# Optimization experiments

Hardware: AMD Instinct MI355X
Metric: run time of the kernel (lower is better)

## Reference

```python
import jax, jax.numpy as jnp
import numpy as np

NUM_CLASSES = 1000
TEMPERATURE = 0.1
B, B_OOD, D = 4096, 4096, 512


def _l2norm(x):
    return x / jnp.linalg.norm(x, axis=-1, keepdims=True)


def setup_inputs() -> dict:
    key = jax.random.key(0)
    k1, k2, k3, k4, k5 = jax.random.split(key, 5)
    return {
        "centers1": _l2norm(jax.random.normal(k1, (NUM_CLASSES, D), dtype=jnp.float32)),
        "features": _l2norm(jax.random.normal(k2, (B, D), dtype=jnp.float32)),
        "targets": jax.random.randint(k3, (B,), 0, NUM_CLASSES, dtype=jnp.int64 if jax.config.jax_enable_x64 else jnp.int32),
        "features_ood": _l2norm(jax.random.normal(k4, (B_OOD, D), dtype=jnp.float32)),
        "pseudo_target_ood": jax.random.randint(k5, (B_OOD,), 0, NUM_CLASSES, dtype=jnp.int64 if jax.config.jax_enable_x64 else jnp.int32),
    }


def reference(centers1, features, targets, features_ood, pseudo_target_ood):
    C = centers1.shape[0]
    b = features.shape[0]
    bo = features_ood.shape[0]
    n = b + C + bo  # total anchors: batch + class centers + ood

    centers_lbl = jnp.arange(C, dtype=targets.dtype)
    ood_lbl = jnp.full((bo,), C, dtype=targets.dtype)  # ood gets label == num_classes
    targets_all = jnp.concatenate([targets, centers_lbl, ood_lbl])              # [N]
    targets_all_class = jnp.concatenate([targets, centers_lbl, pseudo_target_ood])  # [N]

    # per-class count over all N labels (pseudo labels for ood)
    batch_cls_count = jnp.zeros((C,), dtype=jnp.float32).at[targets_all_class].add(1.0)

    # positive mask: same label as anchor, excluding self (diagonal for j < B)
    mask = (targets_all[:b, None] == targets_all[None, :]).astype(jnp.float32)  # [B,N]
    logits_mask = 1.0 - (jnp.arange(n)[None, :] == jnp.arange(b)[:, None]).astype(jnp.float32)
    mask = mask * logits_mask

    features_all = jnp.concatenate([features, centers1, features_ood], axis=0)  # [N,D]
    logits = jnp.matmul(features, features_all.T) / TEMPERATURE                 # [B,N]
    logits = logits - jax.lax.stop_gradient(jnp.max(logits, axis=1, keepdims=True))

    exp_logits = jnp.exp(logits) * logits_mask
    # class-balanced per-instance weight (count of the column's class, minus positive mask)
    per_ins_weight = batch_cls_count[targets_all_class][None, :] - mask         # [B,N]
    exp_logits_sum = jnp.sum(exp_logits / per_ins_weight, axis=1, keepdims=True)
    log_prob = logits - jnp.log(exp_logits_sum)

    mean_log_prob_pos = jnp.sum(mask * log_prob, axis=1) / jnp.sum(mask, axis=1)
    loss = -jnp.mean(mean_log_prob_pos)
    return loss
```

## Files before the change

kernel.cpp:

```cpp
#include <hip/hip_runtime.h>
#include <stdint.h>

#define NUM_C 1000
#define NB    4096
#define NCOL  9192
#define NPAD  9216
#define DK    512
#define BM    128
#define BN    256
#define INV_T 10.0f

typedef __attribute__((ext_vector_type(16))) float f32x16;
typedef __attribute__((ext_vector_type(8)))  int   i32x8;

#define OFF_FALL  0u
#define OFF_CNT   4718592u
#define OFF_CNTT  4722688u
#define OFF_S     4726784u
#define OFF_P     4743168u

__device__ __forceinline__ void async16(const void* g, void* l) {
  __builtin_amdgcn_global_load_lds((const __attribute__((address_space(1))) void*)g,
                                   (__attribute__((address_space(3))) void*)l,
                                   16, 0, 0);
}

__device__ __forceinline__ unsigned sw_e4m3(float x) {
  float ax = fabsf(x);
  unsigned s = (__float_as_uint(x) >> 24) & 0x80u;
  if (ax < 0.015625f) {
    int n = (int)rintf(ax * 512.0f);
    if (n >= 8) return s | 0x08u;
    return s | (unsigned)n;
  }
  if (ax >= 448.0f) return s | 0x7Eu;
  unsigned u = __float_as_uint(ax);
  int ee = (int)(u >> 23) - 127;
  float scale = __uint_as_float((unsigned)(3 - ee + 127) << 23);
  int qv = (int)rintf(ax * scale);
  if (qv == 16) { ee++; qv = 8; }
  return s | (unsigned)(((ee + 7) << 3) | (qv - 8));
}

template <bool HI>
__device__ __forceinline__ int cvt2(float a, float b, int old) {
#if __has_builtin(__builtin_amdgcn_cvt_pk_fp8_f32)
  return __builtin_amdgcn_cvt_pk_fp8_f32(a, b, old, HI);
#else
  unsigned pk = sw_e4m3(a) | (sw_e4m3(b) << 8);
  return HI ? (int)(((unsigned)old & 0x0000FFFFu) | (pk << 16))
            : (int)(((unsigned)old & 0xFFFF0000u) | pk);
#endif
}

__device__ __forceinline__ i32x8 mk8(uint4 lo, uint4 hi) {
  i32x8 r;
  r[0] = (int)lo.x; r[1] = (int)lo.y; r[2] = (int)lo.z; r[3] = (int)lo.w;
  r[4] = (int)hi.x; r[5] = (int)hi.y; r[6] = (int)hi.z; r[7] = (int)hi.w;
  return r;
}

#define MFMA_SC(a, b, c) \
  __builtin_amdgcn_mfma_scale_f32_32x32x64_f8f6f4((a), (b), (c), 0, 0, 0, 0x7F7F7F7F, 0, 0x7F7F7F7F)

__global__ __launch_bounds__(256) void prep_k(const float* __restrict__ centers,
                                              const float* __restrict__ feats,
                                              const float* __restrict__ ood,
                                              const int* __restrict__ targets,
                                              const int* __restrict__ pseudo,
                                              uint4* __restrict__ fall,
                                              unsigned* __restrict__ cnt,
                                              unsigned* __restrict__ cntT,
                                              float* __restrict__ SP) {
  __shared__ unsigned hc[1024];
  __shared__ unsigned hct[1024];
  const int tid = threadIdx.x;

  int idx  = blockIdx.x * 256 + tid;
  int tile = idx >> 10;
  int kq   = (idx >> 7) & 7;
  int p    = idx & 127;
  int c    = p ^ ((p >> 3) & 7);
  int lane = c >> 1;
  int row  = tile * 32 + (lane & 31);
  int k0   = kq * 64 + (lane >> 5) * 32 + (c & 1) * 16;

  const float* src = nullptr;
  if (row < NB)              src = feats   + (size_t)row * DK;
  else if (row < NB + NUM_C) src = centers + (size_t)(row - NB) * DK;
  else if (row < NCOL)       src = ood     + (size_t)(row - NB - NUM_C) * DK;
  uint4 out = make_uint4(0u, 0u, 0u, 0u);
  if (src) {
    float4 v0 = *(const float4*)(src + k0);
    float4 v1 = *(const float4*)(src + k0 + 4);
    float4 v2 = *(const float4*)(src + k0 + 8);
    float4 v3 = *(const float4*)(src + k0 + 12);
    int q;
    q = 0; q = cvt2<false>(v0.x, v0.y, q); q = cvt2<true>(v0.z, v0.w, q); out.x = (unsigned)q;
    q = 0; q = cvt2<false>(v1.x, v1.y, q); q = cvt2<true>(v1.z, v1.w, q); out.y = (unsigned)q;
    q = 0; q = cvt2<false>(v2.x, v2.y, q); q = cvt2<true>(v2.z, v2.w, q); out.z = (unsigned)q;
    q = 0; q = cvt2<false>(v3.x, v3.y, q); q = cvt2<true>(v3.z, v3.w, q); out.w = (unsigned)q;
  }
  fall[idx] = out;

  if (blockIdx.x < 16) {
    for (int kk = tid; kk < 1024; kk += 256) { hc[kk] = 0u; hct[kk] = 0u; }
    __syncthreads();
    int i = blockIdx.x * 256 + tid;
    int tt = targets[i];
    atomicAdd(&hc[tt], 1u);
    atomicAdd(&hct[tt], 1u);
    atomicAdd(&hc[pseudo[i]], 1u);
    __syncthreads();
    for (int kk = tid; kk < 1024; kk += 256) {
      unsigned cc = hc[kk], ct = hct[kk];
      if (cc) atomicAdd(&cnt[kk], cc);
      if (ct) atomicAdd(&cntT[kk], ct);
    }
  } else if (blockIdx.x < 48) {
    SP[(blockIdx.x - 16) * 256 + tid] = 0.0f;
  }
}

__global__ __launch_bounds__(256, 2) void gemm_fused(const unsigned char* __restrict__ fall,
                                                     const int* __restrict__ targets,
                                                     const int* __restrict__ pseudo,
                                                     const unsigned* __restrict__ cnt,
                                                     float* __restrict__ Sacc,
                                                     float* __restrict__ Pacc) {
  __shared__ unsigned char Alds[65536];
  __shared__ int    sLbl[BN];
  __shared__ float  sRw0[BN];
  __shared__ float  sRw1[BN];
  __shared__ int    sTgt[BM];

  const int tid  = threadIdx.x;
  int flat = (int)blockIdx.y * 36 + (int)blockIdx.x;
  int swz  = (flat & 7) * 144 + (flat >> 3);
  const int nTile = swz >> 5;
  const int mTile = swz & 31;
  const int lane  = tid & 63;
  const int wv    = tid >> 6;

  {
    const unsigned char* aSrc = fall + (size_t)mTile * 65536;
#pragma unroll
    for (int i = 0; i < 16; i++)
      async16(aSrc + (i * 256 + tid) * 16, &Alds[(i * 256 + tid) * 16]);
  }

  {
    int j = nTile * BN + tid;
    int lbl, tac;
    if (j >= NCOL)         { lbl = -1; tac = -1; }
    else if (j < NB)       { tac = targets[j]; lbl = tac; }
    else if (j < NB+NUM_C) { tac = j - NB;     lbl = tac; }
    else                   { tac = pseudo[j - NB - NUM_C]; lbl = NUM_C; }
    sLbl[tid] = lbl;
    if (tac >= 0) {
      float w = (float)(1u + cnt[tac]);
      sRw0[tid] = 1.0f / w;
      sRw1[tid] = 1.0f / (w - 1.0f);
    } else {
      sRw0[tid] = 0.f;
      sRw1[tid] = 0.f;
    }
    if (tid < BM) sTgt[tid] = targets[mTile * BM + tid];
  }

  f32x16 acc[4][2];
  {
    f32x16 z;
#pragma unroll
    for (int t = 0; t < 16; t++) z[t] = 0.f;
#pragma unroll
    for (int mi = 0; mi < 4; mi++) { acc[mi][0] = z; acc[mi][1] = z; }
  }

  const int swzo = ((lane >> 2) & 7) << 4;
  const int off0 = (lane << 5) ^ swzo;
  const int off1 = off0 ^ 16;

  const unsigned char* bBase0 = fall + (size_t)(nTile * 8 + wv * 2) * 16384;
  const unsigned char* bBase1 = bBase0 + 16384;

  uint4 b0l = *(const uint4*)(bBase0 + off0);
  uint4 b0h = *(const uint4*)(bBase0 + off1);
  uint4 b1l = *(const uint4*)(bBase1 + off0);
  uint4 b1h = *(const uint4*)(bBase1 + off1);

  __syncthreads();

#pragma unroll
  for (int kq = 0; kq < 8; kq++) {
    uint4 n0l, n0h, n1l, n1h;
    if (kq < 7) {
      const unsigned char* pb0 = bBase0 + (kq + 1) * 2048;
      const unsigned char* pb1 = bBase1 + (kq + 1) * 2048;
      n0l = *(const uint4*)(pb0 + off0); n0h = *(const uint4*)(pb0 + off1);
      n1l = *(const uint4*)(pb1 + off0); n1h = *(const uint4*)(pb1 + off1);
    }
    i32x8 bf0 = mk8(b0l, b0h);
    i32x8 bf1 = mk8(b1l, b1h);
#pragma unroll
    for (int mi = 0; mi < 4; mi++) {
      const unsigned ao = (unsigned)mi * 16384u + (unsigned)kq * 2048u;
      uint4 al = *(const uint4*)&Alds[ao + off0];
      uint4 ah = *(const uint4*)&Alds[ao + off1];
      i32x8 af = mk8(al, ah);
      acc[mi][0] = MFMA_SC(af, bf0, acc[mi][0]);
      acc[mi][1] = MFMA_SC(af, bf1, acc[mi][1]);
    }
    if (kq < 7) { b0l = n0l; b0h = n0h; b1l = n1l; b1h = n1h; }
  }

  const int cq = lane & 31;
  const int hh = lane >> 5;
  const int jl0 = wv * 64 + cq;
  const int jl1 = jl0 + 32;
  const int jg0 = nTile * BN + jl0;
  const int jg1 = jg0 + 32;
  const int lbl0 = sLbl[jl0], lbl1 = sLbl[jl1];
  const float w00 = sRw0[jl0], w01 = sRw1[jl0];
  const float w10 = sRw0[jl1], w11 = sRw1[jl1];

#define RED(m, s, h)                                           \
  {                                                            \
    float sS = (lane & (m)) ? vS[(s)] : vS[(s) + (h)];         \
    float sP = (lane & (m)) ? vP[(s)] : vP[(s) + (h)];         \
    float rS = __shfl_xor(sS, (m), 64);                        \
    float rP = __shfl_xor(sP, (m), 64);                        \
    vS[(s)] = ((lane & (m)) ? vS[(s) + (h)] : vS[(s)]) + rS;   \
    vP[(s)] = ((lane & (m)) ? vP[(s) + (h)] : vP[(s)]) + rP;   \
  }

#pragma unroll
  for (int mi = 0; mi < 4; mi++) {
    float vS[16], vP[16];
#pragma unroll
    for (int r = 0; r < 16; r++) {
      int rowT = (r & 3) + 8 * (r >> 2) + 4 * hh;
      int iloc = mi * 32 + rowT;
      int ig   = mTile * BM + iloc;
      int ti   = sTgt[iloc];
      float l0 = acc[mi][0][r] * INV_T;
      float l1 = acc[mi][1][r] * INV_T;
      bool d0 = (jg0 == ig), d1 = (jg1 == ig);
      bool p0 = (lbl0 == ti) && !d0;
      bool p1 = (lbl1 == ti) && !d1;
      float r0 = d0 ? 0.f : (p0 ? w01 : w00);
      float r1 = d1 ? 0.f : (p1 ? w11 : w10);
      vS[r] = __expf(l0 - 10.0f) * r0 + __expf(l1 - 10.0f) * r1;
      vP[r] = (p0 ? l0 : 0.f) + (p1 ? l1 : 0.f);
    }
    RED(1, 0, 8) RED(1, 1, 8) RED(1, 2, 8) RED(1, 3, 8)
    RED(1, 4, 8) RED(1, 5, 8) RED(1, 6, 8) RED(1, 7, 8)
    RED(2, 0, 4) RED(2, 1, 4) RED(2, 2, 4) RED(2, 3, 4)
    RED(4, 0, 2) RED(4, 1, 2)
    RED(8, 0, 1)
    vS[0] += __shfl_xor(vS[0], 16, 64);
    vP[0] += __shfl_xor(vP[0], 16, 64);
    if (!(lane & 16)) {
      int rr   = ((lane & 1) << 3) | ((lane & 2) << 1) | ((lane & 4) >> 1) | ((lane & 8) >> 3);
      int rowT = (rr & 3) + 8 * (rr >> 2) + 4 * hh;
      int ig   = mTile * BM + mi * 32 + rowT;
      atomicAdd(&Sacc[ig], vS[0]);
      atomicAdd(&Pacc[ig], vP[0]);
    }
  }
#undef RED
}

__global__ __launch_bounds__(256) void finalize_k(const float* __restrict__ S,
                                                  const float* __restrict__ P,
                                                  const int* __restrict__ targets,
                                                  const unsigned* __restrict__ cntT,
                                                  float* __restrict__ out) {
  __shared__ unsigned ct[1024];
  __shared__ float red[4];
  int tid = threadIdx.x;
  for (int k = tid; k < 1024; k += 256) ct[k] = cntT[k];
  __syncthreads();
  float local = 0.f;
  for (int i = tid; i < NB; i += 256) {
    float npos = (float)ct[targets[i]];
    local += P[i] / npos - INV_T - __logf(S[i]);
  }
  for (int m = 1; m < 64; m <<= 1) local += __shfl_xor(local, m, 64);
  if ((tid & 63) == 0) red[tid >> 6] = local;
  __syncthreads();
  if (tid == 0) {
    float t = red[0] + red[1] + red[2] + red[3];
    out[0] = -t / (float)NB;
  }
}

extern "C" void kernel_launch(void* const* d_in, const int* in_sizes, int n_in,
                              void* d_out, int out_size, void* d_ws, size_t ws_size,
                              hipStream_t stream) {
  const float* centers = (const float*)d_in[0];
  const float* feats   = (const float*)d_in[1];
  const int*   targets = (const int*)d_in[2];
  const float* ood     = (const float*)d_in[3];
  const int*   pseudo  = (const int*)d_in[4];

  char* ws = (char*)d_ws;
  uint4*    fall  = (uint4*)(ws + OFF_FALL);
  unsigned* cnt   = (unsigned*)(ws + OFF_CNT);
  unsigned* cntT  = (unsigned*)(ws + OFF_CNTT);
  float*    Sacc  = (float*)(ws + OFF_S);
  float*    Pacc  = (float*)(ws + OFF_P);

  hipMemsetAsync(ws + OFF_CNT, 0, 8192, stream);
  prep_k<<<dim3((NPAD * 32) / 256), 256, 0, stream>>>(centers, feats, ood, targets, pseudo,
                                                      fall, cnt, cntT, Sacc);
  gemm_fused<<<dim3(NPAD / BN, NB / BM), 256, 0, stream>>>((const unsigned char*)fall, targets,
                                                           pseudo, cnt, Sacc, Pacc);
  finalize_k<<<1, 256, 0, stream>>>(Sacc, Pacc, targets, cntT, (float*)d_out);
}
```

Measured before the change: 119.5 us.

## Fold finalize into GEMM via last-block counter, drop memset, use LDS row reduction

Drops the hipMemsetAsync and the separate finalize kernel. The GEMM blocks now bump a global done counter, and the last block to finish computes the loss. The class histogram is built by one dedicated block that writes counts directly, with no global atomics. Per-row partial sums are first reduced in LDS before one global atomic per row, and the MFMA loop runs at raised wave priority. This cuts launch overhead and global atomic traffic, at the cost of a serial single-block histogram and a threadfence per block.

```diff
diff --git a/kernel.cpp b/kernel.cpp
--- a/kernel.cpp
+++ b/kernel.cpp
@@ -18,6 +18,9 @@
 #define OFF_CNTT  4722688u
 #define OFF_S     4726784u
 #define OFF_P     4743168u
+#define OFF_DONE  4759552u
+
+#define NCHUNKBLK 1152
 
 __device__ __forceinline__ void async16(const void* g, void* l) {
   __builtin_amdgcn_global_load_lds((const __attribute__((address_space(1))) void*)g,
@@ -71,54 +74,57 @@
                                               uint4* __restrict__ fall,
                                               unsigned* __restrict__ cnt,
                                               unsigned* __restrict__ cntT,
-                                              float* __restrict__ SP) {
+                                              float* __restrict__ SP,
+                                              unsigned* __restrict__ done) {
   __shared__ unsigned hc[1024];
   __shared__ unsigned hct[1024];
   const int tid = threadIdx.x;
 
-  int idx  = blockIdx.x * 256 + tid;
-  int tile = idx >> 10;
-  int kq   = (idx >> 7) & 7;
-  int p    = idx & 127;
-  int c    = p ^ ((p >> 3) & 7);
-  int lane = c >> 1;
-  int row  = tile * 32 + (lane & 31);
-  int k0   = kq * 64 + (lane >> 5) * 32 + (c & 1) * 16;
-
-  const float* src = nullptr;
-  if (row < NB)              src = feats   + (size_t)row * DK;
-  else if (row < NB + NUM_C) src = centers + (size_t)(row - NB) * DK;
-  else if (row < NCOL)       src = ood     + (size_t)(row - NB - NUM_C) * DK;
-  uint4 out = make_uint4(0u, 0u, 0u, 0u);
-  if (src) {
-    float4 v0 = *(const float4*)(src + k0);
-    float4 v1 = *(const float4*)(src + k0 + 4);
-    float4 v2 = *(const float4*)(src + k0 + 8);
-    float4 v3 = *(const float4*)(src + k0 + 12);
-    int q;
-    q = 0; q = cvt2<false>(v0.x, v0.y, q); q = cvt2<true>(v0.z, v0.w, q); out.x = (unsigned)q;
-    q = 0; q = cvt2<false>(v1.x, v1.y, q); q = cvt2<true>(v1.z, v1.w, q); out.y = (unsigned)q;
-    q = 0; q = cvt2<false>(v2.x, v2.y, q); q = cvt2<true>(v2.z, v2.w, q); out.z = (unsigned)q;
-    q = 0; q = cvt2<false>(v3.x, v3.y, q); q = cvt2<true>(v3.z, v3.w, q); out.w = (unsigned)q;
-  }
-  fall[idx] = out;
-
-  if (blockIdx.x < 16) {
+  if (blockIdx.x < NCHUNKBLK) {
+    int idx  = blockIdx.x * 256 + tid;
+    int tile = idx >> 10;
+    int kq   = (idx >> 7) & 7;
+    int p    = idx & 127;
+    int c    = p ^ ((p >> 3) & 7);
+    int lane = c >> 1;
+    int row  = tile * 32 + (lane & 31);
+    int k0   = kq * 64 + (lane >> 5) * 32 + (c & 1) * 16;
+
+    const float* src = nullptr;
+    if (row < NB)              src = feats   + (size_t)row * DK;
+    else if (row < NB + NUM_C) src = centers + (size_t)(row - NB) * DK;
+    else if (row < NCOL)       src = ood     + (size_t)(row - NB - NUM_C) * DK;
+    uint4 out = make_uint4(0u, 0u, 0u, 0u);
+    if (src) {
+      float4 v0 = *(const float4*)(src + k0);
+      float4 v1 = *(const float4*)(src + k0 + 4);
+      float4 v2 = *(const float4*)(src + k0 + 8);
+      float4 v3 = *(const float4*)(src + k0 + 12);
+      int q;
+      q = 0; q = cvt2<false>(v0.x, v0.y, q); q = cvt2<true>(v0.z, v0.w, q); out.x = (unsigned)q;
+      q = 0; q = cvt2<false>(v1.x, v1.y, q); q = cvt2<true>(v1.z, v1.w, q); out.y = (unsigned)q;
+      q = 0; q = cvt2<false>(v2.x, v2.y, q); q = cvt2<true>(v2.z, v2.w, q); out.z = (unsigned)q;
+      q = 0; q = cvt2<false>(v3.x, v3.y, q); q = cvt2<true>(v3.z, v3.w, q); out.w = (unsigned)q;
+    }
+    fall[idx] = out;
+
+    if (blockIdx.x < 32)
+      SP[blockIdx.x * 256 + tid] = 0.0f;
+  } else {
     for (int kk = tid; kk < 1024; kk += 256) { hc[kk] = 0u; hct[kk] = 0u; }
     __syncthreads();
-    int i = blockIdx.x * 256 + tid;
-    int tt = targets[i];
-    atomicAdd(&hc[tt], 1u);
-    atomicAdd(&hct[tt], 1u);
-    atomicAdd(&hc[pseudo[i]], 1u);
+    for (int i = tid; i < NB; i += 256) {
+      int tt = targets[i];
+      atomicAdd(&hc[tt], 1u);
+      atomicAdd(&hct[tt], 1u);
+      atomicAdd(&hc[pseudo[i]], 1u);
+    }
     __syncthreads();
     for (int kk = tid; kk < 1024; kk += 256) {
-      unsigned cc = hc[kk], ct = hct[kk];
-      if (cc) atomicAdd(&cnt[kk], cc);
-      if (ct) atomicAdd(&cntT[kk], ct);
-    }
-  } else if (blockIdx.x < 48) {
-    SP[(blockIdx.x - 16) * 256 + tid] = 0.0f;
+      cnt[kk]  = hc[kk];
+      cntT[kk] = hct[kk];
+    }
+    if (tid == 0) *done = 0u;
   }
 }
 
@@ -126,13 +132,18 @@
                                                      const int* __restrict__ targets,
                                                      const int* __restrict__ pseudo,
                                                      const unsigned* __restrict__ cnt,
+                                                     const unsigned* __restrict__ cntT,
                                                      float* __restrict__ Sacc,
-                                                     float* __restrict__ Pacc) {
+                                                     float* __restrict__ Pacc,
+                                                     unsigned* __restrict__ done,
+                                                     float* __restrict__ out) {
   __shared__ unsigned char Alds[65536];
   __shared__ int    sLbl[BN];
   __shared__ float  sRw0[BN];
   __shared__ float  sRw1[BN];
   __shared__ int    sTgt[BM];
+  __shared__ unsigned sDone;
+  __shared__ float  red2[4];
 
   const int tid  = threadIdx.x;
   int flat = (int)blockIdx.y * 36 + (int)blockIdx.x;
@@ -191,6 +202,7 @@
 
   __syncthreads();
 
+  __builtin_amdgcn_s_setprio(1);
 #pragma unroll
   for (int kq = 0; kq < 8; kq++) {
     uint4 n0l, n0h, n1l, n1h;
@@ -213,6 +225,7 @@
     }
     if (kq < 7) { b0l = n0l; b0h = n0h; b1l = n1l; b1h = n1h; }
   }
+  __builtin_amdgcn_s_setprio(0);
 
   const int cq = lane & 31;
   const int hh = lane >> 5;
@@ -224,12 +237,18 @@
   const float w00 = sRw0[jl0], w01 = sRw1[jl0];
   const float w10 = sRw0[jl1], w11 = sRw1[jl1];
 
+  float* sS = (float*)Alds;
+  float* sP = (float*)(Alds + 512);
+  __syncthreads();
+  if (tid < BM) { sS[tid] = 0.f; sP[tid] = 0.f; }
+  __syncthreads();
+
 #define RED(m, s, h)                                           \
   {                                                            \
-    float sS = (lane & (m)) ? vS[(s)] : vS[(s) + (h)];         \
-    float sP = (lane & (m)) ? vP[(s)] : vP[(s) + (h)];         \
-    float rS = __shfl_xor(sS, (m), 64);                        \
-    float rP = __shfl_xor(sP, (m), 64);                        \
+    float sSv = (lane & (m)) ? vS[(s)] : vS[(s) + (h)];        \
+    float sPv = (lane & (m)) ? vP[(s)] : vP[(s) + (h)];        \
+    float rS = __shfl_xor(sSv, (m), 64);                       \
+    float rP = __shfl_xor(sPv, (m), 64);                       \
     vS[(s)] = ((lane & (m)) ? vS[(s) + (h)] : vS[(s)]) + rS;   \
     vP[(s)] = ((lane & (m)) ? vP[(s) + (h)] : vP[(s)]) + rP;   \
   }
@@ -258,40 +277,43 @@
     RED(2, 0, 4) RED(2, 1, 4) RED(2, 2, 4) RED(2, 3, 4)
     RED(4, 0, 2) RED(4, 1, 2)
     RED(8, 0, 1)
-    vS[0] += __shfl_xor(vS[0], 16, 64);
-    vP[0] += __shfl_xor(vP[0], 16, 64);
-    if (!(lane & 16)) {
+    {
       int rr   = ((lane & 1) << 3) | ((lane & 2) << 1) | ((lane & 4) >> 1) | ((lane & 8) >> 3);
       int rowT = (rr & 3) + 8 * (rr >> 2) + 4 * hh;
-      int ig   = mTile * BM + mi * 32 + rowT;
-      atomicAdd(&Sacc[ig], vS[0]);
-      atomicAdd(&Pacc[ig], vP[0]);
+      int iloc = mi * 32 + rowT;
+      atomicAdd(&sS[iloc], vS[0]);
+      atomicAdd(&sP[iloc], vP[0]);
     }
   }
 #undef RED
-}
-
-__global__ __launch_bounds__(256) void finalize_k(const float* __restrict__ S,
-                                                  const float* __restrict__ P,
-                                                  const int* __restrict__ targets,
-                                                  const unsigned* __restrict__ cntT,
-                                                  float* __restrict__ out) {
-  __shared__ unsigned ct[1024];
-  __shared__ float red[4];
-  int tid = threadIdx.x;
-  for (int k = tid; k < 1024; k += 256) ct[k] = cntT[k];
-  __syncthreads();
-  float local = 0.f;
-  for (int i = tid; i < NB; i += 256) {
-    float npos = (float)ct[targets[i]];
-    local += P[i] / npos - INV_T - __logf(S[i]);
-  }
-  for (int m = 1; m < 64; m <<= 1) local += __shfl_xor(local, m, 64);
-  if ((tid & 63) == 0) red[tid >> 6] = local;
-  __syncthreads();
-  if (tid == 0) {
-    float t = red[0] + red[1] + red[2] + red[3];
-    out[0] = -t / (float)NB;
+
+  __syncthreads();
+  if (tid < BM) {
+    int ig = mTile * BM + tid;
+    atomicAdd(&Sacc[ig], sS[tid]);
+    atomicAdd(&Pacc[ig], sP[tid]);
+  }
+
+  __threadfence();
+  if (tid == 0) sDone = (atomicAdd(done, 1u) == (unsigned)(36 * 32 - 1)) ? 1u : 0u;
+  __syncthreads();
+  if (sDone) {
+    unsigned* ct = (unsigned*)(Alds + 4096);
+    for (int k = tid; k < 1024; k += 256) ct[k] = cntT[k];
+    __syncthreads();
+    float local = 0.f;
+    for (int i = tid; i < NB; i += 256) {
+      float Sv = atomicAdd(&Sacc[i], 0.0f);
+      float Pv = atomicAdd(&Pacc[i], 0.0f);
+      local += Pv / (float)ct[targets[i]] - INV_T - __logf(Sv);
+    }
+    for (int m = 1; m < 64; m <<= 1) local += __shfl_xor(local, m, 64);
+    if ((tid & 63) == 0) red2[tid >> 6] = local;
+    __syncthreads();
+    if (tid == 0) {
+      float t = red2[0] + red2[1] + red2[2] + red2[3];
+      out[0] = -t / (float)NB;
+    }
   }
 }
 
@@ -310,11 +332,11 @@
   unsigned* cntT  = (unsigned*)(ws + OFF_CNTT);
   float*    Sacc  = (float*)(ws + OFF_S);
   float*    Pacc  = (float*)(ws + OFF_P);
-
-  hipMemsetAsync(ws + OFF_CNT, 0, 8192, stream);
-  prep_k<<<dim3((NPAD * 32) / 256), 256, 0, stream>>>(centers, feats, ood, targets, pseudo,
-                                                      fall, cnt, cntT, Sacc);
+  unsigned* done  = (unsigned*)(ws + OFF_DONE);
+
+  prep_k<<<dim3(NCHUNKBLK + 1), 256, 0, stream>>>(centers, feats, ood, targets, pseudo,
+                                                  fall, cnt, cntT, Sacc, done);
   gemm_fused<<<dim3(NPAD / BN, NB / BM), 256, 0, stream>>>((const unsigned char*)fall, targets,
-                                                           pseudo, cnt, Sacc, Pacc);
-  finalize_k<<<1, 256, 0, stream>>>(Sacc, Pacc, targets, cntT, (float*)d_out);
-}
+                                                           pseudo, cnt, cntT, Sacc, Pacc,
+                                                           done, (float*)d_out);
+}
```

New measurement: 194.9 us. +63.1%, slower.
